# Optimization experiments

Hardware: AMD Instinct MI355X
Metric: run time of the kernel (lower is better)

The kernel has to match this reference:

```python
import jax, jax.numpy as jnp
import numpy as np

N_NODES = 50000
N_EDGES = 800000
IN_FEATS = 128
H_FEATS = 64
NUM_CLASSES = 2
K = 3
LAMBDA_MAX = 2.0  # standard upper bound for normalized-Laplacian max eigenvalue


def setup_inputs() -> dict:
    key = jax.random.key(0)
    ks = jax.random.split(key, 16)
    s = 0.05
    return {
        "in_feat": jax.random.normal(ks[0], (N_NODES, IN_FEATS), jnp.float32),
        "src": jax.random.randint(ks[1], (N_EDGES,), 0, N_NODES, jnp.int32),
        "dst": jax.random.randint(ks[2], (N_EDGES,), 0, N_NODES, jnp.int32),
        "W1": jax.random.normal(ks[3], (H_FEATS, IN_FEATS), jnp.float32) * s,
        "b1": jnp.zeros((H_FEATS,), jnp.float32),
        "W2": jax.random.normal(ks[4], (H_FEATS, H_FEATS), jnp.float32) * s,
        "b2": jnp.zeros((H_FEATS,), jnp.float32),
        "Wc1": jax.random.normal(ks[5], (H_FEATS, K * H_FEATS), jnp.float32) * s,
        "bc1": jnp.zeros((H_FEATS,), jnp.float32),
        "Wc2": jax.random.normal(ks[6], (H_FEATS, K * H_FEATS), jnp.float32) * s,
        "bc2": jnp.zeros((H_FEATS,), jnp.float32),
        "W3": jax.random.normal(ks[7], (H_FEATS, H_FEATS), jnp.float32) * s,
        "b3": jnp.zeros((H_FEATS,), jnp.float32),
        "W4": jax.random.normal(ks[8], (NUM_CLASSES, H_FEATS), jnp.float32) * s,
        "b4": jnp.zeros((NUM_CLASSES,), jnp.float32),
    }


def _cheb_conv(h, src, dst, d_invsqrt, W, b, k):
    """DGL ChebConv: Chebyshev recursion on scaled normalized Laplacian,
    concat k terms along feature dim, then Linear + relu (default activation)."""
    n = h.shape[0]
    re_norm = 2.0 / LAMBDA_MAX

    def a_norm(x):  # D^{-1/2} A D^{-1/2} x via edge-list SpMM
        msg = (x * d_invsqrt)[src]                              # [E, F]
        agg = jax.ops.segment_sum(msg, dst, num_segments=n)     # [N, F]
        return agg * d_invsqrt

    X0 = h
    Xs = [X0]
    X1 = -re_norm * a_norm(X0) + X0 * (re_norm - 1.0)
    Xs.append(X1)
    for _ in range(2, k):
        Xi = -2.0 * re_norm * a_norm(X1) + X1 * (2.0 * (re_norm - 1.0)) - X0
        Xs.append(Xi)
        X0, X1 = X1, Xi
    Xt = jnp.concatenate(Xs, axis=1)                            # [N, k*F]
    return jax.nn.relu(Xt @ W.T + b)


def reference(in_feat, src, dst, W1, b1, W2, b2, Wc1, bc1, Wc2, bc2, W3, b3, W4, b4):
    n = in_feat.shape[0]
    # in-degrees from dst, clamp(min=1), D^{-1/2}
    deg = jax.ops.segment_sum(jnp.ones_like(dst, jnp.float32), dst, num_segments=n)
    d_invsqrt = jnp.power(jnp.maximum(deg, 1.0), -0.5)[:, None]  # [N, 1]

    h = jax.nn.relu(in_feat @ W1.T + b1)
    h = jax.nn.relu(h @ W2.T + b2)
    h = _cheb_conv(h, src, dst, d_invsqrt, Wc1, bc1, K)
    h = _cheb_conv(h, src, dst, d_invsqrt, Wc2, bc2, K)
    h = jax.nn.relu(h @ W3.T + b3)
    h = h @ W4.T + b4
    return h
```

## Files before the change

kernel.cpp:

```cpp
#include <hip/hip_runtime.h>
#include <hip/hip_fp16.h>
#include <math.h>

#define NN 50000
#define NE 800000
#define INF 128
#define H 64
#define ELLCAP 64
#define NB_G ((NN + 63) / 64)
#define WOFF_W1 0
#define WOFF_W2 8192
#define WOFF_WC1 12288
#define WOFF_WC2 24576
#define WOFF_W3 36864
#define WTOT 40960
#define NB_CVTW (WTOT / 2048)

#define PSHIFT 8
#define NPART2 196
#define CAP 8192
#define NB_BINA 128
#define EPB (NE / NB_BINA)
#define EPT_A 25

#define TSCALE 64.0f
#define TSCALE_INV 0.015625f

typedef _Float16 half8_t __attribute__((ext_vector_type(8)));
typedef float float4_t __attribute__((ext_vector_type(4)));
typedef float float2_t __attribute__((ext_vector_type(2)));

__device__ __forceinline__ half8_t load_cvt8(const float* p) {
  float4 a = *(const float4*)(p);
  float4 b = *(const float4*)(p + 4);
  half8_t h;
  h[0] = (_Float16)a.x; h[1] = (_Float16)a.y; h[2] = (_Float16)a.z; h[3] = (_Float16)a.w;
  h[4] = (_Float16)b.x; h[5] = (_Float16)b.y; h[6] = (_Float16)b.z; h[7] = (_Float16)b.w;
  return h;
}

__device__ __forceinline__ unsigned char enc1(float x) {
  return (unsigned char)(__builtin_amdgcn_cvt_pk_fp8_f32(x, x, 0u, false) & 0xFFu);
}
__device__ __forceinline__ unsigned int enc4(float a, float b, float c, float d) {
  unsigned int v = __builtin_amdgcn_cvt_pk_fp8_f32(a, b, 0u, false);
  v = __builtin_amdgcn_cvt_pk_fp8_f32(c, d, v, true);
  return v;
}
__device__ __forceinline__ void dec8(unsigned int lo, unsigned int hi, float* f) {
  float2_t a = __builtin_amdgcn_cvt_pk_f32_fp8(lo, false);
  float2_t b = __builtin_amdgcn_cvt_pk_f32_fp8(lo, true);
  float2_t c = __builtin_amdgcn_cvt_pk_f32_fp8(hi, false);
  float2_t d = __builtin_amdgcn_cvt_pk_f32_fp8(hi, true);
  f[0] = a[0]; f[1] = a[1]; f[2] = b[0]; f[3] = b[1];
  f[4] = c[0]; f[5] = c[1]; f[6] = d[0]; f[7] = d[1];
}

__global__ __launch_bounds__(256) void k_binA(const int* __restrict__ src, const int* __restrict__ dst,
                                              int* __restrict__ gcount, int* __restrict__ bucket,
                                              const float* __restrict__ W1, const float* __restrict__ W2,
                                              const float* __restrict__ Wc1, const float* __restrict__ Wc2,
                                              const float* __restrict__ W3, _Float16* __restrict__ w16) {
  int b = blockIdx.x;
  if (b >= NB_BINA) {
    int i0 = (b - NB_BINA) * 2048 + threadIdx.x * 8;
#pragma unroll
    for (int k = 0; k < 8; ++k) {
      int id = i0 + k;
      if (id < WTOT) {
        float v;
        if (id < WOFF_W2) v = W1[id];
        else if (id < WOFF_WC1) v = W2[id - WOFF_W2];
        else if (id < WOFF_WC2) v = Wc1[id - WOFF_WC1];
        else if (id < WOFF_W3) v = Wc2[id - WOFF_WC2];
        else v = W3[id - WOFF_W3];
        w16[id] = (_Float16)v;
      }
    }
    return;
  }
  __shared__ int s_cnt[NPART2];
  __shared__ int s_base[NPART2];
  const int tid = threadIdx.x;
  if (tid < NPART2) s_cnt[tid] = 0;
  __syncthreads();
  const int e0 = b * EPB;
  int rec[EPT_A];
  int meta[EPT_A];
#pragma unroll
  for (int i = 0; i < EPT_A; ++i) {
    int off = i * 256 + tid;
    meta[i] = -1;
    if (off < EPB) {
      int e = e0 + off;
      int d = __builtin_nontemporal_load(&dst[e]);
      int s = __builtin_nontemporal_load(&src[e]);
      int p = d >> PSHIFT;
      rec[i] = s | ((d & 255) << 16);
      int slot = atomicAdd(&s_cnt[p], 1);
      meta[i] = (p << 13) | slot;
    }
  }
  __syncthreads();
  if (tid < NPART2) s_base[tid] = atomicAdd(&gcount[tid], s_cnt[tid]);
  __syncthreads();
#pragma unroll
  for (int i = 0; i < EPT_A; ++i) {
    if (meta[i] >= 0) {
      int p = meta[i] >> 13;
      int pos = s_base[p] + (meta[i] & 8191);
      if (pos < CAP) bucket[(size_t)p * CAP + pos] = rec[i];
    }
  }
}

__global__ __launch_bounds__(256) void k_binB(const int* __restrict__ gcount, const int* __restrict__ bucket,
                                              unsigned short* __restrict__ ell, int* __restrict__ cnt,
                                              float* __restrict__ dinv32) {
  __shared__ int s_cnt[256];
  const int tid = threadIdx.x;
  const int p = blockIdx.x;
  s_cnt[tid] = 0;
  __syncthreads();
  int n = gcount[p];
  n = n < CAP ? n : CAP;
  const int* bp = bucket + (size_t)p * CAP;
  int j = tid;
  for (; j + 3 * 256 < n; j += 4 * 256) {
    int r0 = bp[j], r1 = bp[j + 256], r2 = bp[j + 512], r3 = bp[j + 768];
    int c0 = atomicAdd(&s_cnt[r0 >> 16], 1);
    int c1 = atomicAdd(&s_cnt[r1 >> 16], 1);
    int c2 = atomicAdd(&s_cnt[r2 >> 16], 1);
    int c3 = atomicAdd(&s_cnt[r3 >> 16], 1);
    if (c0 < ELLCAP) ell[((size_t)((p << PSHIFT) + (r0 >> 16)) << 6) + c0] = (unsigned short)(r0 & 0xFFFF);
    if (c1 < ELLCAP) ell[((size_t)((p << PSHIFT) + (r1 >> 16)) << 6) + c1] = (unsigned short)(r1 & 0xFFFF);
    if (c2 < ELLCAP) ell[((size_t)((p << PSHIFT) + (r2 >> 16)) << 6) + c2] = (unsigned short)(r2 & 0xFFFF);
    if (c3 < ELLCAP) ell[((size_t)((p << PSHIFT) + (r3 >> 16)) << 6) + c3] = (unsigned short)(r3 & 0xFFFF);
  }
  for (; j < n; j += 256) {
    int r = bp[j];
    int dl = r >> 16;
    int c = atomicAdd(&s_cnt[dl], 1);
    if (c < ELLCAP) ell[((size_t)((p << PSHIFT) + dl) << 6) + c] = (unsigned short)(r & 0xFFFF);
  }
  __syncthreads();
  int node = (p << PSHIFT) + tid;
  if (node < NN) {
    int c = s_cnt[tid];
    cnt[node] = c;
    dinv32[node] = 1.0f / sqrtf((float)(c < 1 ? 1 : c));
  }
}

__global__ __launch_bounds__(256) void k_mlp(const float* __restrict__ in_feat,
                                             const _Float16* __restrict__ w16,
                                             const float* __restrict__ b1,
                                             const float* __restrict__ b2,
                                             const float* __restrict__ dinv32,
                                             _Float16* __restrict__ X0c,
                                             unsigned char* __restrict__ X0t, int N) {
  __shared__ _Float16 Hs[64][72];
  const int tid = threadIdx.x;
  const int wave = tid >> 6;
  const int lane = tid & 63;
  const int m = lane & 15;
  const int quad = lane >> 4;
  const int rbase = blockIdx.x * 64 + wave * 16;
  int arow = rbase + m;
  arow = arow < N ? arow : N - 1;
  const float* Ap = in_feat + (size_t)arow * INF + quad * 8;
  const _Float16* B1 = w16 + WOFF_W1 + (size_t)m * INF + quad * 8;
  float4_t acc[4] = {{0.f,0.f,0.f,0.f},{0.f,0.f,0.f,0.f},{0.f,0.f,0.f,0.f},{0.f,0.f,0.f,0.f}};
#pragma unroll
  for (int k0 = 0; k0 < INF; k0 += 32) {
    half8_t a = load_cvt8(Ap + k0);
    half8_t b0 = *(const half8_t*)(B1 + k0);
    half8_t b1f = *(const half8_t*)(B1 + 16 * INF + k0);
    half8_t b2f = *(const half8_t*)(B1 + 32 * INF + k0);
    half8_t b3f = *(const half8_t*)(B1 + 48 * INF + k0);
    acc[0] = __builtin_amdgcn_mfma_f32_16x16x32_f16(a, b0, acc[0], 0, 0, 0);
    acc[1] = __builtin_amdgcn_mfma_f32_16x16x32_f16(a, b1f, acc[1], 0, 0, 0);
    acc[2] = __builtin_amdgcn_mfma_f32_16x16x32_f16(a, b2f, acc[2], 0, 0, 0);
    acc[3] = __builtin_amdgcn_mfma_f32_16x16x32_f16(a, b3f, acc[3], 0, 0, 0);
  }
#pragma unroll
  for (int i = 0; i < 4; ++i)
#pragma unroll
    for (int t = 0; t < 4; ++t)
      Hs[wave * 16 + quad * 4 + i][t * 16 + m] = (_Float16)fmaxf(acc[t][i] + b1[t * 16 + m], 0.f);
  __syncthreads();
  const _Float16* Ap2 = &Hs[wave * 16 + m][quad * 8];
  const _Float16* B2 = w16 + WOFF_W2 + (size_t)m * H + quad * 8;
  float4_t acc2[4] = {{0.f,0.f,0.f,0.f},{0.f,0.f,0.f,0.f},{0.f,0.f,0.f,0.f},{0.f,0.f,0.f,0.f}};
#pragma unroll
  for (int k0 = 0; k0 < H; k0 += 32) {
    half8_t a = *(const half8_t*)(Ap2 + k0);
    half8_t b0 = *(const half8_t*)(B2 + k0);
    half8_t b1f = *(const half8_t*)(B2 + 16 * H + k0);
    half8_t b2f = *(const half8_t*)(B2 + 32 * H + k0);
    half8_t b3f = *(const half8_t*)(B2 + 48 * H + k0);
    acc2[0] = __builtin_amdgcn_mfma_f32_16x16x32_f16(a, b0, acc2[0], 0, 0, 0);
    acc2[1] = __builtin_amdgcn_mfma_f32_16x16x32_f16(a, b1f, acc2[1], 0, 0, 0);
    acc2[2] = __builtin_amdgcn_mfma_f32_16x16x32_f16(a, b2f, acc2[2], 0, 0, 0);
    acc2[3] = __builtin_amdgcn_mfma_f32_16x16x32_f16(a, b3f, acc2[3], 0, 0, 0);
  }
#pragma unroll
  for (int i = 0; i < 4; ++i) {
    int rr = rbase + quad * 4 + i;
    if (rr < N) {
      float dn = TSCALE * dinv32[rr];
#pragma unroll
      for (int t = 0; t < 4; ++t) {
        float v = fmaxf(acc2[t][i] + b2[t * 16 + m], 0.f);
        X0c[((size_t)rr << 6) + t * 16 + m] = (_Float16)v;
        X0t[((size_t)rr << 6) + t * 16 + m] = enc1(dn * v);
      }
    }
  }
}

__global__ __launch_bounds__(256) void k_spmm(const unsigned char* __restrict__ tabs,
                                              const _Float16* __restrict__ auxc,
                                              _Float16* __restrict__ outc,
                                              unsigned char* __restrict__ outt,
                                              const int* __restrict__ cnt,
                                              const float* __restrict__ dinv32,
                                              const unsigned short* __restrict__ ell,
                                              float alpha, int use_aux, int N) {
  int wv = (blockIdx.x * 256 + threadIdx.x) >> 6;
  int lane = threadIdx.x & 63;
  int node = wv * 8 + (lane >> 3);
  if (node >= N) return;
  int c8 = (lane & 7) * 8;
  int deg0 = cnt[node];
  int deg = deg0 < ELLCAP ? deg0 : ELLCAP;
  const unsigned short* row = ell + ((size_t)node << 6);

  float acc[8] = {0.f, 0.f, 0.f, 0.f, 0.f, 0.f, 0.f, 0.f};
  float f[8];
  int j = 0;
  for (; j + 7 < deg; j += 8) {
    ushort4 ra = *(const ushort4*)(row + j);
    ushort4 rb = *(const ushort4*)(row + j + 4);
    uint2 q0 = *(const uint2*)(tabs + (((size_t)ra.x) << 6) + c8);
    uint2 q1 = *(const uint2*)(tabs + (((size_t)ra.y) << 6) + c8);
    uint2 q2 = *(const uint2*)(tabs + (((size_t)ra.z) << 6) + c8);
    uint2 q3 = *(const uint2*)(tabs + (((size_t)ra.w) << 6) + c8);
    uint2 q4 = *(const uint2*)(tabs + (((size_t)rb.x) << 6) + c8);
    uint2 q5 = *(const uint2*)(tabs + (((size_t)rb.y) << 6) + c8);
    uint2 q6 = *(const uint2*)(tabs + (((size_t)rb.z) << 6) + c8);
    uint2 q7 = *(const uint2*)(tabs + (((size_t)rb.w) << 6) + c8);
    dec8(q0.x, q0.y, f);
#pragma unroll
    for (int k = 0; k < 8; ++k) acc[k] += f[k];
    dec8(q1.x, q1.y, f);
#pragma unroll
    for (int k = 0; k < 8; ++k) acc[k] += f[k];
    dec8(q2.x, q2.y, f);
#pragma unroll
    for (int k = 0; k < 8; ++k) acc[k] += f[k];
    dec8(q3.x, q3.y, f);
#pragma unroll
    for (int k = 0; k < 8; ++k) acc[k] += f[k];
    dec8(q4.x, q4.y, f);
#pragma unroll
    for (int k = 0; k < 8; ++k) acc[k] += f[k];
    dec8(q5.x, q5.y, f);
#pragma unroll
    for (int k = 0; k < 8; ++k) acc[k] += f[k];
    dec8(q6.x, q6.y, f);
#pragma unroll
    for (int k = 0; k < 8; ++k) acc[k] += f[k];
    dec8(q7.x, q7.y, f);
#pragma unroll
    for (int k = 0; k < 8; ++k) acc[k] += f[k];
  }
  for (; j + 3 < deg; j += 4) {
    ushort4 ra = *(const ushort4*)(row + j);
    uint2 q0 = *(const uint2*)(tabs + (((size_t)ra.x) << 6) + c8);
    uint2 q1 = *(const uint2*)(tabs + (((size_t)ra.y) << 6) + c8);
    uint2 q2 = *(const uint2*)(tabs + (((size_t)ra.z) << 6) + c8);
    uint2 q3 = *(const uint2*)(tabs + (((size_t)ra.w) << 6) + c8);
    dec8(q0.x, q0.y, f);
#pragma unroll
    for (int k = 0; k < 8; ++k) acc[k] += f[k];
    dec8(q1.x, q1.y, f);
#pragma unroll
    for (int k = 0; k < 8; ++k) acc[k] += f[k];
    dec8(q2.x, q2.y, f);
#pragma unroll
    for (int k = 0; k < 8; ++k) acc[k] += f[k];
    dec8(q3.x, q3.y, f);
#pragma unroll
    for (int k = 0; k < 8; ++k) acc[k] += f[k];
  }
  for (; j < deg; ++j) {
    size_t s = row[j];
    uint2 q0 = *(const uint2*)(tabs + (s << 6) + c8);
    dec8(q0.x, q0.y, f);
#pragma unroll
    for (int k = 0; k < 8; ++k) acc[k] += f[k];
  }
  float dn = dinv32[node];
  float a = alpha * dn * TSCALE_INV;
  float r[8];
#pragma unroll
  for (int k = 0; k < 8; ++k) r[k] = a * acc[k];
  if (use_aux) {
    half8_t x = *(const half8_t*)(auxc + ((size_t)node << 6) + c8);
#pragma unroll
    for (int k = 0; k < 8; ++k) r[k] -= (float)x[k];
  }
  half8_t ro;
#pragma unroll
  for (int k = 0; k < 8; ++k) ro[k] = (_Float16)r[k];
  *(half8_t*)(outc + ((size_t)node << 6) + c8) = ro;
  if (outt) {
    float sc = TSCALE * dn;
    uint2 q;
    q.x = enc4(sc * r[0], sc * r[1], sc * r[2], sc * r[3]);
    q.y = enc4(sc * r[4], sc * r[5], sc * r[6], sc * r[7]);
    *(uint2*)(outt + ((size_t)node << 6) + c8) = q;
  }
}

__global__ __launch_bounds__(256) void k_gemm192(const _Float16* __restrict__ A0,
                                                 const _Float16* __restrict__ A1,
                                                 const _Float16* __restrict__ A2,
                                                 const _Float16* __restrict__ B,
                                                 const float* __restrict__ bias,
                                                 const float* __restrict__ dinv32,
                                                 _Float16* __restrict__ outc,
                                                 unsigned char* __restrict__ outt, int N) {
  const int tid = threadIdx.x;
  const int wave = tid >> 6;
  const int lane = tid & 63;
  const int m = lane & 15;
  const int quad = lane >> 4;
  const int rbase = blockIdx.x * 64 + wave * 16;
  int arow = rbase + m;
  arow = arow < N ? arow : N - 1;
  const size_t ro = ((size_t)arow << 6) + quad * 8;
  const _Float16* Bp = B + (size_t)m * 192 + quad * 8;
  float4_t acc[4] = {{0.f,0.f,0.f,0.f},{0.f,0.f,0.f,0.f},{0.f,0.f,0.f,0.f},{0.f,0.f,0.f,0.f}};
#pragma unroll
  for (int k0 = 0; k0 < 192; k0 += 32) {
    half8_t a;
    if (k0 < 64) a = *(const half8_t*)(A0 + ro + k0);
    else if (k0 < 128) a = *(const half8_t*)(A1 + ro + (k0 - 64));
    else a = *(const half8_t*)(A2 + ro + (k0 - 128));
    half8_t b0 = *(const half8_t*)(Bp + k0);
    half8_t b1f = *(const half8_t*)(Bp + 16 * 192 + k0);
    half8_t b2f = *(const half8_t*)(Bp + 32 * 192 + k0);
    half8_t b3f = *(const half8_t*)(Bp + 48 * 192 + k0);
    acc[0] = __builtin_amdgcn_mfma_f32_16x16x32_f16(a, b0, acc[0], 0, 0, 0);
    acc[1] = __builtin_amdgcn_mfma_f32_16x16x32_f16(a, b1f, acc[1], 0, 0, 0);
    acc[2] = __builtin_amdgcn_mfma_f32_16x16x32_f16(a, b2f, acc[2], 0, 0, 0);
    acc[3] = __builtin_amdgcn_mfma_f32_16x16x32_f16(a, b3f, acc[3], 0, 0, 0);
  }
#pragma unroll
  for (int i = 0; i < 4; ++i) {
    int rr = rbase + quad * 4 + i;
    if (rr < N) {
      float dn = TSCALE * dinv32[rr];
#pragma unroll
      for (int t = 0; t < 4; ++t) {
        float v = fmaxf(acc[t][i] + bias[t * 16 + m], 0.f);
        outc[((size_t)rr << 6) + t * 16 + m] = (_Float16)v;
        outt[((size_t)rr << 6) + t * 16 + m] = enc1(dn * v);
      }
    }
  }
}

__global__ __launch_bounds__(256) void k_tail(const _Float16* __restrict__ A0,
                                              const _Float16* __restrict__ A1,
                                              const _Float16* __restrict__ A2,
                                              const _Float16* __restrict__ w16,
                                              const float* __restrict__ bc2,
                                              const float* __restrict__ b3,
                                              const float* __restrict__ W4,
                                              const float* __restrict__ b4,
                                              float* __restrict__ out, int N) {
  __shared__ _Float16 Hs2[64][72];
  __shared__ float Hs3[64][65];
  const int tid = threadIdx.x;
  const int wave = tid >> 6;
  const int lane = tid & 63;
  const int m = lane & 15;
  const int quad = lane >> 4;
  const int rbase = blockIdx.x * 64 + wave * 16;
  int arow = rbase + m;
  arow = arow < N ? arow : N - 1;
  {
    const size_t ro = ((size_t)arow << 6) + quad * 8;
    const _Float16* Bp = w16 + WOFF_WC2 + (size_t)m * 192 + quad * 8;
    float4_t acc[4] = {{0.f,0.f,0.f,0.f},{0.f,0.f,0.f,0.f},{0.f,0.f,0.f,0.f},{0.f,0.f,0.f,0.f}};
#pragma unroll
    for (int k0 = 0; k0 < 192; k0 += 32) {
      half8_t a;
      if (k0 < 64) a = *(const half8_t*)(A0 + ro + k0);
      else if (k0 < 128) a = *(const half8_t*)(A1 + ro + (k0 - 64));
      else a = *(const half8_t*)(A2 + ro + (k0 - 128));
      half8_t b0 = *(const half8_t*)(Bp + k0);
      half8_t b1f = *(const half8_t*)(Bp + 16 * 192 + k0);
      half8_t b2f = *(const half8_t*)(Bp + 32 * 192 + k0);
      half8_t b3f = *(const half8_t*)(Bp + 48 * 192 + k0);
      acc[0] = __builtin_amdgcn_mfma_f32_16x16x32_f16(a, b0, acc[0], 0, 0, 0);
      acc[1] = __builtin_amdgcn_mfma_f32_16x16x32_f16(a, b1f, acc[1], 0, 0, 0);
      acc[2] = __builtin_amdgcn_mfma_f32_16x16x32_f16(a, b2f, acc[2], 0, 0, 0);
      acc[3] = __builtin_amdgcn_mfma_f32_16x16x32_f16(a, b3f, acc[3], 0, 0, 0);
    }
#pragma unroll
    for (int i = 0; i < 4; ++i)
#pragma unroll
      for (int t = 0; t < 4; ++t)
        Hs2[wave * 16 + quad * 4 + i][t * 16 + m] =
            (_Float16)fmaxf(acc[t][i] + bc2[t * 16 + m], 0.f);
  }
  __syncthreads();
  {
    const _Float16* Ap = &Hs2[wave * 16 + m][quad * 8];
    const _Float16* Bp = w16 + WOFF_W3 + (size_t)m * H + quad * 8;
    float4_t acc[4] = {{0.f,0.f,0.f,0.f},{0.f,0.f,0.f,0.f},{0.f,0.f,0.f,0.f},{0.f,0.f,0.f,0.f}};
#pragma unroll
    for (int k0 = 0; k0 < H; k0 += 32) {
      half8_t a = *(const half8_t*)(Ap + k0);
      half8_t b0 = *(const half8_t*)(Bp + k0);
      half8_t b1f = *(const half8_t*)(Bp + 16 * H + k0);
      half8_t b2f = *(const half8_t*)(Bp + 32 * H + k0);
      half8_t b3f = *(const half8_t*)(Bp + 48 * H + k0);
      acc[0] = __builtin_amdgcn_mfma_f32_16x16x32_f16(a, b0, acc[0], 0, 0, 0);
      acc[1] = __builtin_amdgcn_mfma_f32_16x16x32_f16(a, b1f, acc[1], 0, 0, 0);
      acc[2] = __builtin_amdgcn_mfma_f32_16x16x32_f16(a, b2f, acc[2], 0, 0, 0);
      acc[3] = __builtin_amdgcn_mfma_f32_16x16x32_f16(a, b3f, acc[3], 0, 0, 0);
    }
#pragma unroll
    for (int i = 0; i < 4; ++i)
#pragma unroll
      for (int t = 0; t < 4; ++t)
        Hs3[wave * 16 + quad * 4 + i][t * 16 + m] = fmaxf(acc[t][i] + b3[t * 16 + m], 0.f);
  }
  __syncthreads();
  if (tid < 128) {
    int r = tid >> 1;
    int c = tid & 1;
    int row = blockIdx.x * 64 + r;
    if (row < N) {
      const float* w4 = W4 + c * 64;
      float s = 0.f;
#pragma unroll
      for (int k = 0; k < 64; ++k) s = fmaf(Hs3[r][k], w4[k], s);
      out[(size_t)row * 2 + c] = s + b4[c];
    }
  }
}

extern "C" void kernel_launch(void* const* d_in, const int* in_sizes, int n_in,
                              void* d_out, int out_size, void* d_ws, size_t ws_size,
                              hipStream_t stream) {
  const float* in_feat = (const float*)d_in[0];
  const int* src = (const int*)d_in[1];
  const int* dst = (const int*)d_in[2];
  const float* W1 = (const float*)d_in[3];
  const float* b1 = (const float*)d_in[4];
  const float* W2 = (const float*)d_in[5];
  const float* b2 = (const float*)d_in[6];
  const float* Wc1 = (const float*)d_in[7];
  const float* bc1 = (const float*)d_in[8];
  const float* Wc2 = (const float*)d_in[9];
  const float* bc2 = (const float*)d_in[10];
  const float* W3 = (const float*)d_in[11];
  const float* b3 = (const float*)d_in[12];
  const float* W4 = (const float*)d_in[13];
  const float* b4 = (const float*)d_in[14];
  float* out = (float*)d_out;

  char* ws = (char*)d_ws;
  size_t o = 0;
  auto carve = [&](size_t bytes) -> void* {
    o = (o + 255) & ~(size_t)255;
    void* p = ws + o;
    o += bytes;
    return p;
  };
  int* cnt = (int*)carve((size_t)NN * 4);
  unsigned short* ell = (unsigned short*)carve((size_t)NN * ELLCAP * 2);
  float* dinv32 = (float*)carve((size_t)NN * 4);
  _Float16* w16 = (_Float16*)carve((size_t)WTOT * 2);
  _Float16* X0c = (_Float16*)carve((size_t)NN * H * 2);
  unsigned char* X0t = (unsigned char*)carve((size_t)NN * H);
  _Float16* X1c = (_Float16*)carve((size_t)NN * H * 2);
  unsigned char* X1t = (unsigned char*)carve((size_t)NN * H);
  _Float16* X2c = (_Float16*)carve((size_t)NN * H * 2);
  _Float16* Y0c = (_Float16*)carve((size_t)NN * H * 2);
  unsigned char* Y0t = (unsigned char*)carve((size_t)NN * H);
  _Float16* Y1c = (_Float16*)carve((size_t)NN * H * 2);
  unsigned char* Y1t = (unsigned char*)carve((size_t)NN * H);
  _Float16* Y2c = (_Float16*)carve((size_t)NN * H * 2);
  int* gcount = (int*)carve((size_t)NPART2 * 4);
  int* bucket = (int*)Y0c;
  (void)ws_size; (void)in_sizes; (void)n_in; (void)out_size;

  const int NB_S = (NN + 31) / 32;

  hipMemsetAsync(gcount, 0, (size_t)NPART2 * 4, stream);
  k_binA<<<NB_BINA + NB_CVTW, 256, 0, stream>>>(src, dst, gcount, bucket, W1, W2, Wc1, Wc2, W3, w16);
  k_binB<<<NPART2, 256, 0, stream>>>(gcount, bucket, ell, cnt, dinv32);
  k_mlp<<<NB_G, 256, 0, stream>>>(in_feat, w16, b1, b2, dinv32, X0c, X0t, NN);
  k_spmm<<<NB_S, 256, 0, stream>>>(X0t, (const _Float16*)nullptr, X1c, X1t, cnt, dinv32, ell, -1.f, 0, NN);
  k_spmm<<<NB_S, 256, 0, stream>>>(X1t, X0c, X2c, (unsigned char*)nullptr, cnt, dinv32, ell, -2.f, 1, NN);
  k_gemm192<<<NB_G, 256, 0, stream>>>(X0c, X1c, X2c, w16 + WOFF_WC1, bc1, dinv32, Y0c, Y0t, NN);
  k_spmm<<<NB_S, 256, 0, stream>>>(Y0t, (const _Float16*)nullptr, Y1c, Y1t, cnt, dinv32, ell, -1.f, 0, NN);
  k_spmm<<<NB_S, 256, 0, stream>>>(Y1t, Y0c, Y2c, (unsigned char*)nullptr, cnt, dinv32, ell, -2.f, 1, NN);
  k_tail<<<NB_G, 256, 0, stream>>>(Y0c, Y1c, Y2c, w16, bc2, b3, W4, b4, out, NN);
}
```

Measured before the change: 227.5 us.

## Fuse second Chebyshev SpMM into the following GEMM kernels via shared memory

The second SpMM of each ChebConv (the X2/Y2 term) is computed inside the consuming GEMM kernel. Each block gathers the fp8 neighbour rows for its 64 nodes into an LDS tile, which then feeds the last K-slice of the MFMA GEMM. This drops two kernel launches and the fp16 X2/Y2 round trip through global memory. In exchange, the gather runs at 64 threads per block-row with 16-byte loads, so it has less parallelism and memory-level concurrency than the standalone SpMM, and the GEMM waits on a barrier behind it.

```diff
diff --git a/kernel.cpp b/kernel.cpp
--- a/kernel.cpp
+++ b/kernel.cpp
@@ -54,6 +54,10 @@
   float2_t d = __builtin_amdgcn_cvt_pk_f32_fp8(hi, true);
   f[0] = a[0]; f[1] = a[1]; f[2] = b[0]; f[3] = b[1];
   f[4] = c[0]; f[5] = c[1]; f[6] = d[0]; f[7] = d[1];
+}
+__device__ __forceinline__ void dec16(uint4 q, float* f) {
+  dec8(q.x, q.y, f);
+  dec8(q.z, q.w, f + 8);
 }
 
 __global__ __launch_bounds__(256) void k_binA(const int* __restrict__ src, const int* __restrict__ dst,
@@ -220,13 +224,11 @@
 }
 
 __global__ __launch_bounds__(256) void k_spmm(const unsigned char* __restrict__ tabs,
-                                              const _Float16* __restrict__ auxc,
                                               _Float16* __restrict__ outc,
                                               unsigned char* __restrict__ outt,
                                               const int* __restrict__ cnt,
                                               const float* __restrict__ dinv32,
-                                              const unsigned short* __restrict__ ell,
-                                              float alpha, int use_aux, int N) {
+                                              const unsigned short* __restrict__ ell, int N) {
   int wv = (blockIdx.x * 256 + threadIdx.x) >> 6;
   int lane = threadIdx.x & 63;
   int node = wv * 8 + (lane >> 3);
@@ -302,39 +304,94 @@
     for (int k = 0; k < 8; ++k) acc[k] += f[k];
   }
   float dn = dinv32[node];
-  float a = alpha * dn * TSCALE_INV;
+  float a = -dn * TSCALE_INV;
   float r[8];
 #pragma unroll
   for (int k = 0; k < 8; ++k) r[k] = a * acc[k];
-  if (use_aux) {
-    half8_t x = *(const half8_t*)(auxc + ((size_t)node << 6) + c8);
-#pragma unroll
-    for (int k = 0; k < 8; ++k) r[k] -= (float)x[k];
-  }
   half8_t ro;
 #pragma unroll
   for (int k = 0; k < 8; ++k) ro[k] = (_Float16)r[k];
   *(half8_t*)(outc + ((size_t)node << 6) + c8) = ro;
-  if (outt) {
-    float sc = TSCALE * dn;
-    uint2 q;
-    q.x = enc4(sc * r[0], sc * r[1], sc * r[2], sc * r[3]);
-    q.y = enc4(sc * r[4], sc * r[5], sc * r[6], sc * r[7]);
-    *(uint2*)(outt + ((size_t)node << 6) + c8) = q;
-  }
-}
-
-__global__ __launch_bounds__(256) void k_gemm192(const _Float16* __restrict__ A0,
-                                                 const _Float16* __restrict__ A1,
-                                                 const _Float16* __restrict__ A2,
-                                                 const _Float16* __restrict__ B,
-                                                 const float* __restrict__ bias,
-                                                 const float* __restrict__ dinv32,
-                                                 _Float16* __restrict__ outc,
-                                                 unsigned char* __restrict__ outt, int N) {
+  float sc = TSCALE * dn;
+  uint2 q;
+  q.x = enc4(sc * r[0], sc * r[1], sc * r[2], sc * r[3]);
+  q.y = enc4(sc * r[4], sc * r[5], sc * r[6], sc * r[7]);
+  *(uint2*)(outt + ((size_t)node << 6) + c8) = q;
+}
+
+__global__ __launch_bounds__(256) void k_gemmX2(const unsigned char* __restrict__ tabs,
+                                                const _Float16* __restrict__ A0,
+                                                const _Float16* __restrict__ A1,
+                                                const _Float16* __restrict__ B,
+                                                const float* __restrict__ bias,
+                                                const float* __restrict__ dinv32,
+                                                const int* __restrict__ cnt,
+                                                const unsigned short* __restrict__ ell,
+                                                _Float16* __restrict__ outc,
+                                                unsigned char* __restrict__ outt, int N) {
+  __shared__ _Float16 X2s[64][72];
   const int tid = threadIdx.x;
   const int wave = tid >> 6;
   const int lane = tid & 63;
+  {
+    int lrow = wave * 16 + (lane >> 2);
+    int gnode = blockIdx.x * 64 + lrow;
+    int gc = (lane & 3) * 16;
+    float a16[16];
+#pragma unroll
+    for (int k = 0; k < 16; ++k) a16[k] = 0.f;
+    int deg = 0;
+    if (gnode < N) {
+      int d0 = cnt[gnode];
+      deg = d0 < ELLCAP ? d0 : ELLCAP;
+    }
+    const unsigned short* row = ell + ((size_t)gnode << 6);
+    float f[16];
+    int j = 0;
+    for (; j + 3 < deg; j += 4) {
+      ushort4 ra = *(const ushort4*)(row + j);
+      uint4 q0 = *(const uint4*)(tabs + (((size_t)ra.x) << 6) + gc);
+      uint4 q1 = *(const uint4*)(tabs + (((size_t)ra.y) << 6) + gc);
+      uint4 q2 = *(const uint4*)(tabs + (((size_t)ra.z) << 6) + gc);
+      uint4 q3 = *(const uint4*)(tabs + (((size_t)ra.w) << 6) + gc);
+      dec16(q0, f);
+#pragma unroll
+      for (int k = 0; k < 16; ++k) a16[k] += f[k];
+      dec16(q1, f);
+#pragma unroll
+      for (int k = 0; k < 16; ++k) a16[k] += f[k];
+      dec16(q2, f);
+#pragma unroll
+      for (int k = 0; k < 16; ++k) a16[k] += f[k];
+      dec16(q3, f);
+#pragma unroll
+      for (int k = 0; k < 16; ++k) a16[k] += f[k];
+    }
+    for (; j < deg; ++j) {
+      size_t s = row[j];
+      uint4 q0 = *(const uint4*)(tabs + (s << 6) + gc);
+      dec16(q0, f);
+#pragma unroll
+      for (int k = 0; k < 16; ++k) a16[k] += f[k];
+    }
+    half8_t o0, o1;
+    if (gnode < N) {
+      float aa = -2.f * dinv32[gnode] * TSCALE_INV;
+      half8_t x0a = *(const half8_t*)(A0 + ((size_t)gnode << 6) + gc);
+      half8_t x0b = *(const half8_t*)(A0 + ((size_t)gnode << 6) + gc + 8);
+#pragma unroll
+      for (int k = 0; k < 8; ++k) {
+        o0[k] = (_Float16)(aa * a16[k] - (float)x0a[k]);
+        o1[k] = (_Float16)(aa * a16[k + 8] - (float)x0b[k]);
+      }
+    } else {
+#pragma unroll
+      for (int k = 0; k < 8; ++k) { o0[k] = (_Float16)0.f; o1[k] = (_Float16)0.f; }
+    }
+    *(half8_t*)(&X2s[lrow][gc]) = o0;
+    *(half8_t*)(&X2s[lrow][gc + 8]) = o1;
+  }
+  __syncthreads();
   const int m = lane & 15;
   const int quad = lane >> 4;
   const int rbase = blockIdx.x * 64 + wave * 16;
@@ -348,7 +405,7 @@
     half8_t a;
     if (k0 < 64) a = *(const half8_t*)(A0 + ro + k0);
     else if (k0 < 128) a = *(const half8_t*)(A1 + ro + (k0 - 64));
-    else a = *(const half8_t*)(A2 + ro + (k0 - 128));
+    else a = *(const half8_t*)(&X2s[wave * 16 + m][quad * 8 + (k0 - 128)]);
     half8_t b0 = *(const half8_t*)(Bp + k0);
     half8_t b1f = *(const half8_t*)(Bp + 16 * 192 + k0);
     half8_t b2f = *(const half8_t*)(Bp + 32 * 192 + k0);
@@ -373,20 +430,83 @@
   }
 }
 
-__global__ __launch_bounds__(256) void k_tail(const _Float16* __restrict__ A0,
-                                              const _Float16* __restrict__ A1,
-                                              const _Float16* __restrict__ A2,
-                                              const _Float16* __restrict__ w16,
-                                              const float* __restrict__ bc2,
-                                              const float* __restrict__ b3,
-                                              const float* __restrict__ W4,
-                                              const float* __restrict__ b4,
-                                              float* __restrict__ out, int N) {
+__global__ __launch_bounds__(256) void k_tail2(const unsigned char* __restrict__ tabs,
+                                               const _Float16* __restrict__ A0,
+                                               const _Float16* __restrict__ A1,
+                                               const _Float16* __restrict__ w16,
+                                               const float* __restrict__ bc2,
+                                               const float* __restrict__ b3,
+                                               const float* __restrict__ W4,
+                                               const float* __restrict__ b4,
+                                               const float* __restrict__ dinv32,
+                                               const int* __restrict__ cnt,
+                                               const unsigned short* __restrict__ ell,
+                                               float* __restrict__ out, int N) {
+  __shared__ _Float16 Y2s[64][72];
   __shared__ _Float16 Hs2[64][72];
   __shared__ float Hs3[64][65];
   const int tid = threadIdx.x;
   const int wave = tid >> 6;
   const int lane = tid & 63;
+  {
+    int lrow = wave * 16 + (lane >> 2);
+    int gnode = blockIdx.x * 64 + lrow;
+    int gc = (lane & 3) * 16;
+    float a16[16];
+#pragma unroll
+    for (int k = 0; k < 16; ++k) a16[k] = 0.f;
+    int deg = 0;
+    if (gnode < N) {
+      int d0 = cnt[gnode];
+      deg = d0 < ELLCAP ? d0 : ELLCAP;
+    }
+    const unsigned short* row = ell + ((size_t)gnode << 6);
+    float f[16];
+    int j = 0;
+    for (; j + 3 < deg; j += 4) {
+      ushort4 ra = *(const ushort4*)(row + j);
+      uint4 q0 = *(const uint4*)(tabs + (((size_t)ra.x) << 6) + gc);
+      uint4 q1 = *(const uint4*)(tabs + (((size_t)ra.y) << 6) + gc);
+      uint4 q2 = *(const uint4*)(tabs + (((size_t)ra.z) << 6) + gc);
+      uint4 q3 = *(const uint4*)(tabs + (((size_t)ra.w) << 6) + gc);
+      dec16(q0, f);
+#pragma unroll
+      for (int k = 0; k < 16; ++k) a16[k] += f[k];
+      dec16(q1, f);
+#pragma unroll
+      for (int k = 0; k < 16; ++k) a16[k] += f[k];
+      dec16(q2, f);
+#pragma unroll
+      for (int k = 0; k < 16; ++k) a16[k] += f[k];
+      dec16(q3, f);
+#pragma unroll
+      for (int k = 0; k < 16; ++k) a16[k] += f[k];
+    }
+    for (; j < deg; ++j) {
+      size_t s = row[j];
+      uint4 q0 = *(const uint4*)(tabs + (s << 6) + gc);
+      dec16(q0, f);
+#pragma unroll
+      for (int k = 0; k < 16; ++k) a16[k] += f[k];
+    }
+    half8_t o0, o1;
+    if (gnode < N) {
+      float aa = -2.f * dinv32[gnode] * TSCALE_INV;
+      half8_t y0a = *(const half8_t*)(A0 + ((size_t)gnode << 6) + gc);
+      half8_t y0b = *(const half8_t*)(A0 + ((size_t)gnode << 6) + gc + 8);
+#pragma unroll
+      for (int k = 0; k < 8; ++k) {
+        o0[k] = (_Float16)(aa * a16[k] - (float)y0a[k]);
+        o1[k] = (_Float16)(aa * a16[k + 8] - (float)y0b[k]);
+      }
+    } else {
+#pragma unroll
+      for (int k = 0; k < 8; ++k) { o0[k] = (_Float16)0.f; o1[k] = (_Float16)0.f; }
+    }
+    *(half8_t*)(&Y2s[lrow][gc]) = o0;
+    *(half8_t*)(&Y2s[lrow][gc + 8]) = o1;
+  }
+  __syncthreads();
   const int m = lane & 15;
   const int quad = lane >> 4;
   const int rbase = blockIdx.x * 64 + wave * 16;
@@ -401,7 +521,7 @@
       half8_t a;
       if (k0 < 64) a = *(const half8_t*)(A0 + ro + k0);
       else if (k0 < 128) a = *(const half8_t*)(A1 + ro + (k0 - 64));
-      else a = *(const half8_t*)(A2 + ro + (k0 - 128));
+      else a = *(const half8_t*)(&Y2s[wave * 16 + m][quad * 8 + (k0 - 128)]);
       half8_t b0 = *(const half8_t*)(Bp + k0);
       half8_t b1f = *(const half8_t*)(Bp + 16 * 192 + k0);
       half8_t b2f = *(const half8_t*)(Bp + 32 * 192 + k0);
@@ -492,12 +612,10 @@
   unsigned char* X0t = (unsigned char*)carve((size_t)NN * H);
   _Float16* X1c = (_Float16*)carve((size_t)NN * H * 2);
   unsigned char* X1t = (unsigned char*)carve((size_t)NN * H);
-  _Float16* X2c = (_Float16*)carve((size_t)NN * H * 2);
   _Float16* Y0c = (_Float16*)carve((size_t)NN * H * 2);
   unsigned char* Y0t = (unsigned char*)carve((size_t)NN * H);
   _Float16* Y1c = (_Float16*)carve((size_t)NN * H * 2);
   unsigned char* Y1t = (unsigned char*)carve((size_t)NN * H);
-  _Float16* Y2c = (_Float16*)carve((size_t)NN * H * 2);
   int* gcount = (int*)carve((size_t)NPART2 * 4);
   int* bucket = (int*)Y0c;
   (void)ws_size; (void)in_sizes; (void)n_in; (void)out_size;
@@ -508,10 +626,8 @@
   k_binA<<<NB_BINA + NB_CVTW, 256, 0, stream>>>(src, dst, gcount, bucket, W1, W2, Wc1, Wc2, W3, w16);
   k_binB<<<NPART2, 256, 0, stream>>>(gcount, bucket, ell, cnt, dinv32);
   k_mlp<<<NB_G, 256, 0, stream>>>(in_feat, w16, b1, b2, dinv32, X0c, X0t, NN);
-  k_spmm<<<NB_S, 256, 0, stream>>>(X0t, (const _Float16*)nullptr, X1c, X1t, cnt, dinv32, ell, -1.f, 0, NN);
-  k_spmm<<<NB_S, 256, 0, stream>>>(X1t, X0c, X2c, (unsigned char*)nullptr, cnt, dinv32, ell, -2.f, 1, NN);
-  k_gemm192<<<NB_G, 256, 0, stream>>>(X0c, X1c, X2c, w16 + WOFF_WC1, bc1, dinv32, Y0c, Y0t, NN);
-  k_spmm<<<NB_S, 256, 0, stream>>>(Y0t, (const _Float16*)nullptr, Y1c, Y1t, cnt, dinv32, ell, -1.f, 0, NN);
-  k_spmm<<<NB_S, 256, 0, stream>>>(Y1t, Y0c, Y2c, (unsigned char*)nullptr, cnt, dinv32, ell, -2.f, 1, NN);
-  k_tail<<<NB_G, 256, 0, stream>>>(Y0c, Y1c, Y2c, w16, bc2, b3, W4, b4, out, NN);
-}
+  k_spmm<<<NB_S, 256, 0, stream>>>(X0t, X1c, X1t, cnt, dinv32, ell, NN);
+  k_gemmX2<<<NB_G, 256, 0, stream>>>(X1t, X0c, X1c, w16 + WOFF_WC1, bc1, dinv32, cnt, ell, Y0c, Y0t, NN);
+  k_spmm<<<NB_S, 256, 0, stream>>>(Y0t, Y1c, Y1t, cnt, dinv32, ell, NN);
+  k_tail2<<<NB_G, 256, 0, stream>>>(Y1t, Y0c, Y1c, w16, bc2, b3, W4, b4, dinv32, cnt, ell, out, NN);
+}
```

Measured after the change: 225.9 us. No clear change (-0.7%).
